# Optimization experiments

Hardware: AMD Instinct MI355X
Metric: run time of the kernel (lower is better)

The kernel has to match this reference:

```python
import jax, jax.numpy as jnp
import numpy as np

SEQ, B, I, H, STEPS = 512, 64, 512, 512, 5


def _lin_init(key, out_dim, in_dim):
    k1, k2 = jax.random.split(key)
    bound = 1.0 / np.sqrt(in_dim)
    W = jax.random.uniform(k1, (out_dim, in_dim), jnp.float32, -bound, bound)
    b = jax.random.uniform(k2, (out_dim,), jnp.float32, -bound, bound)
    return W, b


def _make_layer(key, in_size, hid):
    ks = jax.random.split(key, STEPS + 2)
    mogW, mogb = [], []
    for i in range(STEPS):
        # even i: Linear(hidden -> input) applied to h; odd i: Linear(input -> hidden) applied to x
        out_d, in_d = (in_size, hid) if i % 2 == 0 else (hid, in_size)
        W, b = _lin_init(ks[i], out_d, in_d)
        mogW.append(W); mogb.append(b)
    Wih, bih = _lin_init(ks[STEPS], 4 * hid, in_size)
    Whh, bhh = _lin_init(ks[STEPS + 1], 4 * hid, hid)
    return jnp.stack(mogW), jnp.stack(mogb), Wih, Whh, bih, bhh


def setup_inputs() -> dict:
    key = jax.random.key(0)
    kx, k1, k2 = jax.random.split(key, 3)
    inp = {"input_seq": jax.random.normal(kx, (SEQ, B, I), jnp.float32)}
    l1 = _make_layer(k1, I, H)
    l2 = _make_layer(k2, H, H)
    for pfx, p in (("l1", l1), ("l2", l2)):
        for nm, arr in zip(("mogW", "mogb", "Wih", "Whh", "bih", "bhh"), p):
            inp[f"{pfx}_{nm}"] = arr
    return inp


def _mog_cell(x, h, c, mogW, mogb, Wih, Whh, bih, bhh):
    # mogrify: 5 alternating gated linear updates
    for i in range(STEPS):
        if i % 2 == 0:
            x = 2.0 * jax.nn.sigmoid(h @ mogW[i].T + mogb[i]) * x
        else:
            h = 2.0 * jax.nn.sigmoid(x @ mogW[i].T + mogb[i]) * h
    # LSTMCell (PyTorch gate order: i, f, g, o)
    gates = x @ Wih.T + bih + h @ Whh.T + bhh
    ig, fg, gg, og = jnp.split(gates, 4, axis=-1)
    c = jax.nn.sigmoid(fg) * c + jax.nn.sigmoid(ig) * jnp.tanh(gg)
    h = jax.nn.sigmoid(og) * jnp.tanh(c)
    return h, c


def reference(input_seq, l1_mogW, l1_mogb, l1_Wih, l1_Whh, l1_bih, l1_bhh,
              l2_mogW, l2_mogb, l2_Wih, l2_Whh, l2_bih, l2_bhh):
    batch = input_seq.shape[1]
    h1 = jnp.zeros((batch, H), input_seq.dtype)
    c1 = jnp.zeros_like(h1); h2 = jnp.zeros_like(h1); c2 = jnp.zeros_like(h1)

    def step(carry, x_t):
        h1, c1, h2, c2 = carry
        h1, c1 = _mog_cell(x_t, h1, c1, l1_mogW, l1_mogb, l1_Wih, l1_Whh, l1_bih, l1_bhh)
        h2, c2 = _mog_cell(h1, h2, c2, l2_mogW, l2_mogb, l2_Wih, l2_Whh, l2_bih, l2_bhh)
        return (h1, c1, h2, c2), h2

    (h1, c1, h2, c2), outputs = jax.lax.scan(step, (h1, c1, h2, c2), input_seq)
    last_hidden = jnp.stack([h1, h2])  # [2, B, H]
    last_cell = jnp.stack([c1, c2])
    return outputs, last_hidden, last_cell
```

## Files before the change

kernel.cpp:

```cpp
#include <hip/hip_runtime.h>
#include <cstdint>

#define SEQ   512
#define BATCH 64
#define HID   512
#define BH    (BATCH*HID)
#define NWGP  32
#define NTHR  256

#define MOG_ELEMS   (5*512*512)
#define GATE_ELEMS  (2048*512)
#define LAYER_ELEMS (MOG_ELEMS + 2*GATE_ELEMS)

#define WS_FLG   0
#define WS_H16   4096
#define ZERO_PREFIX 266240
#define WS_X16   266240
#define WS_RING  397312
#define WS_WT    921600

#define OUT_H 16777216
#define OUT_C 16842752

typedef _Float16 f16x8 __attribute__((ext_vector_type(8)));
typedef float    f32x4 __attribute__((ext_vector_type(4)));

#define MFMA(a,b,c) __builtin_amdgcn_mfma_f32_16x16x32_f16((a),(b),(c),0,0,0)

#define GLD16(dst, ptr) \
    asm volatile("global_load_dwordx4 %0, %1, off sc0 sc1" : "=v"(dst) : "v"(ptr))
#define GLDF(dst, ptr) \
    asm volatile("global_load_dword %0, %1, off sc0 sc1" : "=v"(dst) : "v"(ptr))
#define GST16(ptr, val) \
    asm volatile("global_store_dwordx4 %0, %1, off sc0 sc1" :: "v"(ptr), "v"(val) : "memory")
#define FLAGST(ptr, val) \
    asm volatile("global_store_dword %0, %1, off sc0 sc1" :: "v"(ptr), "v"(val) : "memory")
#define VMWAIT() asm volatile("s_waitcnt vmcnt(0)" ::: "memory")

__device__ __forceinline__ float sigf(float z) { return 1.f / (1.f + __expf(-z)); }

__device__ __forceinline__ void poll_ge(const unsigned* line, unsigned tag) {
    if (threadIdx.x < 64) {
        const unsigned* p = line + (threadIdx.x & 31);
        for (;;) {
            unsigned v;
            asm volatile("global_load_dword %0, %1, off sc0 sc1\n\ts_waitcnt vmcnt(0)"
                         : "=v"(v) : "v"(p) : "memory");
            if (__ballot(v >= tag) == ~0ull) break;
        }
    }
    __syncthreads();
}

__device__ __forceinline__ int gate_orig_row(int rg) {
    return ((rg >> 4) & 3) * 512 + ((rg >> 6) << 4) + (rg & 15);
}

__global__ __launch_bounds__(256)
void prologue_convert(const float* __restrict__ l1_mogW, const float* __restrict__ l1_Wih,
                      const float* __restrict__ l1_Whh,
                      const float* __restrict__ l2_mogW, const float* __restrict__ l2_Wih,
                      const float* __restrict__ l2_Whh,  char* __restrict__ ws)
{
    _Float16* wdst = (_Float16*)(ws + WS_WT);
    const int total = 2 * LAYER_ELEMS;
    const int stride = gridDim.x * blockDim.x;
    for (int idx = blockIdx.x * blockDim.x + threadIdx.x; idx < total; idx += stride) {
        const int layer = idx >= LAYER_ELEMS;
        const int r = idx - layer * LAYER_ELEMS;
        float v;
        if (r < MOG_ELEMS) {
            v = (layer ? l2_mogW : l1_mogW)[r];
        } else {
            const int q = r - MOG_ELEMS;
            const int mat = q >= GATE_ELEMS;
            const int e = q - mat * GATE_ELEMS;
            const int rg = e >> 9;
            const int k  = e & 511;
            const int orig = gate_orig_row(rg);
            const float* W = mat ? (layer ? l2_Whh : l1_Whh)
                                 : (layer ? l2_Wih : l1_Wih);
            v = W[orig * 512 + k];
        }
        wdst[idx] = (_Float16)v;
    }
}

__global__ __launch_bounds__(NTHR, 1)
void moglstm_persist(const float* __restrict__ in_seq,
                     const float* __restrict__ mogb1, const float* __restrict__ mogb2,
                     const float* __restrict__ bih1,  const float* __restrict__ bhh1,
                     const float* __restrict__ bih2,  const float* __restrict__ bhh2,
                     float* __restrict__ out, char* __restrict__ ws)
{
    const int pool = blockIdx.x >> 5;
    const int w    = blockIdx.x & 31;
    const int tid  = threadIdx.x;
    const int lane = tid & 63;
    const int wv   = tid >> 6;

    extern __shared__ char smem[];
    _Float16* wlds = (_Float16*)smem;
    _Float16* hbuf = (_Float16*)(smem + 81920);
    float*    fbuf = (float*)(smem + 84992);

    unsigned* flg     = (unsigned*)(ws + WS_FLG);
    unsigned* myline  = flg + (pool * 6) * 32;
    unsigned* othline = flg + ((1 - pool) * 6) * 32;

    _Float16* h16 = (_Float16*)(ws + WS_H16) + pool * (2 * BH);
    _Float16* x16 = (_Float16*)(ws + WS_X16) + pool * BH;
    float*    ring = (float*)(ws + WS_RING);
    const _Float16* Wb   = (const _Float16*)(ws + WS_WT) + (size_t)pool * LAYER_ELEMS;
    const _Float16* mogW = Wb;
    const _Float16* wihR = Wb + MOG_ELEMS;
    const _Float16* whhR = wihR + GATE_ELEMS;
    const float* mogb = pool ? mogb2 : mogb1;
    const float* bih  = pool ? bih2 : bih1;
    const float* bhh  = pool ? bhh2 : bhh1;

    const int j     = lane & 15;
    const int hi    = lane >> 4;
    const int kof   = hi * 8;
    const int arow  = 16 * wv + j;
    const int erow0 = 16 * wv + 4 * hi;
    const int ecol  = 16 * w + j;
    const int cxor  = (j & 7) << 3;
    const int aoff  = (hi >> 1) * 1024 + arow * 16 + (hi & 1) * 8;

    for (int i = tid; i < 5 * 16 * 64; i += NTHR) {
        const int p   = i >> 10;
        const int rem = i & 1023;
        const int c   = rem >> 6;
        const int k   = (rem & 63) << 3;
        f16x8 v = *(const f16x8*)(mogW + ((size_t)p * 512 + 16 * w + c) * 512 + k);
        *(f16x8*)&wlds[((p * 16 + c) << 9) + (k ^ ((c & 7) << 3))] = v;
    }
    __syncthreads();

    float mb[5];
    #pragma unroll
    for (int p = 0; p < 5; ++p) mb[p] = mogb[p * 512 + ecol];
    float gbias[4];
    #pragma unroll
    for (int g = 0; g < 4; ++g) gbias[g] = bih[g * 512 + ecol] + bhh[g * 512 + ecol];

    float xreg[4];
    float hreg[4] = {0.f, 0.f, 0.f, 0.f};
    float creg[4] = {0.f, 0.f, 0.f, 0.f};

    for (int t = 0; t < SEQ; ++t) {
        _Float16* hb = h16 + (t & 1) * BH;
        _Float16* ho = h16 + ((t & 1) ^ 1) * BH;

        float xseq[4];
        if (pool == 0) {
            #pragma unroll
            for (int r = 0; r < 4; ++r)
                xseq[r] = in_seq[(size_t)t * BH + (erow0 + r) * HID + ecol];
        }

        #pragma unroll
        for (int p = 0; p < 5; ++p) {
            if (p == 0) {
                if (t > 0) poll_ge(myline + 5 * 32, 6u * (t - 1) + 6);
                if (pool == 1) poll_ge(othline + 5 * 32, 6u * t + 6);
            } else {
                poll_ge(myline + (p - 1) * 32, 6u * t + p);
            }

            const _Float16* act = (p & 1) ? x16 : hb;

            float rv[4];
            if (p == 0 && pool == 1) {
                const float* rp = ring + (t & 3) * BH + w * 1024 + erow0 * 16 + j;
                GLDF(rv[0], rp); GLDF(rv[1], rp + 16); GLDF(rv[2], rp + 32); GLDF(rv[3], rp + 48);
            }
            f16x8 a[16];
            {
                const _Float16* ab = act + aoff;
                #pragma unroll
                for (int ks = 0; ks < 16; ++ks) GLD16(a[ks], ab + ks * 2048);
            }
            VMWAIT();
            __builtin_amdgcn_sched_barrier(0);

            const _Float16* wl = wlds + ((p * 16 + j) << 9);
            f32x4 acc = {0.f, 0.f, 0.f, 0.f};
            #pragma unroll
            for (int ks = 0; ks < 16; ++ks)
                acc = MFMA(a[ks], *(const f16x8*)&wl[(kof + ks * 32) ^ cxor], acc);

            float nv[4];
            #pragma unroll
            for (int r = 0; r < 4; ++r) {
                const float s = 2.f * sigf(acc[r] + mb[p]);
                if ((p & 1) == 0) {
                    const float xo = (p == 0) ? ((pool == 0) ? xseq[r] : rv[r]) : xreg[r];
                    nv[r] = s * xo;  xreg[r] = nv[r];
                } else {
                    nv[r] = s * hreg[r];  hreg[r] = nv[r];
                }
            }
            _Float16* target = ((p & 1) == 0) ? x16 : hb;
            #pragma unroll
            for (int r = 0; r < 4; ++r) hbuf[(erow0 + r) * 24 + j] = (_Float16)nv[r];
            __syncthreads();
            if (tid < 128) {
                const int row = tid >> 1, c8 = (tid & 1) * 8;
                f16x8 v = *(const f16x8*)&hbuf[row * 24 + c8];
                GST16(target + w * 1024 + row * 16 + c8, v);
            }
            VMWAIT();
            __syncthreads();
            if (tid == 0) FLAGST(myline + p * 32 + w, 6u * t + p + 1);
        }

        poll_ge(myline + 4 * 32, 6u * t + 5);
        if (pool == 0 && t >= 4) poll_ge(othline + 0 * 32, 6u * (t - 4) + 1);

        f16x8 ax[16], ah[16];
        {
            const _Float16* xb = x16 + aoff;
            const _Float16* hB = hb  + aoff;
            #pragma unroll
            for (int ks = 0; ks < 16; ++ks) { GLD16(ax[ks], xb + ks * 2048); GLD16(ah[ks], hB + ks * 2048); }
        }
        VMWAIT();
        __builtin_amdgcn_sched_barrier(0);

        f32x4 g0 = {0,0,0,0}, g1 = {0,0,0,0}, g2 = {0,0,0,0}, g3 = {0,0,0,0};
        {
            const int n0 = 64 * w + j;
            const _Float16* bi0 = wihR + (size_t)(n0     ) * 512 + kof;
            const _Float16* bi1 = wihR + (size_t)(n0 + 16) * 512 + kof;
            const _Float16* bi2 = wihR + (size_t)(n0 + 32) * 512 + kof;
            const _Float16* bi3 = wihR + (size_t)(n0 + 48) * 512 + kof;
            const _Float16* bh0 = whhR + (size_t)(n0     ) * 512 + kof;
            const _Float16* bh1 = whhR + (size_t)(n0 + 16) * 512 + kof;
            const _Float16* bh2 = whhR + (size_t)(n0 + 32) * 512 + kof;
            const _Float16* bh3 = whhR + (size_t)(n0 + 48) * 512 + kof;
            #pragma unroll
            for (int ks = 0; ks < 16; ++ks) {
                const int o = ks * 32;
                g0 = MFMA(ax[ks], *(const f16x8*)(bi0 + o), g0);
                g0 = MFMA(ah[ks], *(const f16x8*)(bh0 + o), g0);
                g1 = MFMA(ax[ks], *(const f16x8*)(bi1 + o), g1);
                g1 = MFMA(ah[ks], *(const f16x8*)(bh1 + o), g1);
                g2 = MFMA(ax[ks], *(const f16x8*)(bi2 + o), g2);
                g2 = MFMA(ah[ks], *(const f16x8*)(bh2 + o), g2);
                g3 = MFMA(ax[ks], *(const f16x8*)(bi3 + o), g3);
                g3 = MFMA(ah[ks], *(const f16x8*)(bh3 + o), g3);
            }
        }
        float hnv[4], cnv[4];
        #pragma unroll
        for (int r = 0; r < 4; ++r) {
            const float ig = sigf (g0[r] + gbias[0]);
            const float fg = sigf (g1[r] + gbias[1]);
            const float gg = tanhf(g2[r] + gbias[2]);
            const float og = sigf (g3[r] + gbias[3]);
            const float cn = fg * creg[r] + ig * gg;
            creg[r] = cn;  cnv[r] = cn;
            const float hn = og * tanhf(cn);
            hreg[r] = hn;  hnv[r] = hn;
        }
        #pragma unroll
        for (int r = 0; r < 4; ++r) hbuf[(erow0 + r) * 24 + j] = (_Float16)hnv[r];
        if (pool == 0) {
            #pragma unroll
            for (int r = 0; r < 4; ++r) fbuf[(erow0 + r) * 20 + j] = hnv[r];
        } else {
            #pragma unroll
            for (int r = 0; r < 4; ++r)
                out[(size_t)t * BH + (erow0 + r) * HID + ecol] = hnv[r];
        }
        if (t == SEQ - 1) {
            #pragma unroll
            for (int r = 0; r < 4; ++r) {
                out[OUT_H + pool * BH + (erow0 + r) * HID + ecol] = hnv[r];
                out[OUT_C + pool * BH + (erow0 + r) * HID + ecol] = cnv[r];
            }
        }
        __syncthreads();
        if (tid < 128) {
            const int row = tid >> 1, c8 = (tid & 1) * 8;
            f16x8 v = *(const f16x8*)&hbuf[row * 24 + c8];
            GST16(ho + w * 1024 + row * 16 + c8, v);
        }
        if (pool == 0) {
            const int row = tid >> 2, c4 = (tid & 3) * 4;
            f32x4 v = *(const f32x4*)&fbuf[row * 20 + c4];
            GST16(ring + (t & 3) * BH + w * 1024 + row * 16 + c4, v);
        }
        VMWAIT();
        __syncthreads();
        if (tid == 0) FLAGST(myline + 5 * 32 + w, 6u * t + 6);
    }
}

extern "C" void kernel_launch(void* const* d_in, const int* in_sizes, int n_in,
                              void* d_out, int out_size, void* d_ws, size_t ws_size,
                              hipStream_t stream) {
    const float* in_seq  = (const float*)d_in[0];
    const float* l1_mogW = (const float*)d_in[1];
    const float* l1_mogb = (const float*)d_in[2];
    const float* l1_Wih  = (const float*)d_in[3];
    const float* l1_Whh  = (const float*)d_in[4];
    const float* l1_bih  = (const float*)d_in[5];
    const float* l1_bhh  = (const float*)d_in[6];
    const float* l2_mogW = (const float*)d_in[7];
    const float* l2_mogb = (const float*)d_in[8];
    const float* l2_Wih  = (const float*)d_in[9];
    const float* l2_Whh  = (const float*)d_in[10];
    const float* l2_bih  = (const float*)d_in[11];
    const float* l2_bhh  = (const float*)d_in[12];

    hipMemsetAsync(d_ws, 0, ZERO_PREFIX, stream);

    prologue_convert<<<256, 256, 0, stream>>>(l1_mogW, l1_Wih, l1_Whh,
                                              l2_mogW, l2_Wih, l2_Whh, (char*)d_ws);

    moglstm_persist<<<64, NTHR, 90112, stream>>>(in_seq, l1_mogb, l2_mogb,
                                                 l1_bih, l1_bhh, l2_bih, l2_bhh,
                                                 (float*)d_out, (char*)d_ws);
}
```

Before: 17.43 ms.

## Speculatively load activations while polling flags, split gate MFMAs across phases

Replaces the poll-then-syncthreads barrier with a loop in which every wave issues its activation loads together with the flag load, repeating until a poll after the flags are satisfied, so no separate barrier and load round trip is needed. Flags are spread to one per 64-byte slot (larger flag region, shifted workspace offsets). The recurrent Whh half of the LSTM gate GEMM is folded into the last mogrifier phase using the h already in registers, so the final stage only reloads x. Output stores become nontemporal. The extra speculative reload adds memory traffic, and correctness depends on the final load being ordered after the flag observation.

```diff
diff --git a/kernel.cpp b/kernel.cpp
--- a/kernel.cpp
+++ b/kernel.cpp
@@ -13,11 +13,11 @@
 #define LAYER_ELEMS (MOG_ELEMS + 2*GATE_ELEMS)
 
 #define WS_FLG   0
-#define WS_H16   4096
-#define ZERO_PREFIX 266240
-#define WS_X16   266240
-#define WS_RING  397312
-#define WS_WT    921600
+#define WS_H16   24576
+#define ZERO_PREFIX 286720
+#define WS_X16   286720
+#define WS_RING  417792
+#define WS_WT    942080
 
 #define OUT_H 16777216
 #define OUT_C 16842752
@@ -36,21 +36,12 @@
 #define FLAGST(ptr, val) \
     asm volatile("global_store_dword %0, %1, off sc0 sc1" :: "v"(ptr), "v"(val) : "memory")
 #define VMWAIT() asm volatile("s_waitcnt vmcnt(0)" ::: "memory")
+#define TIE(x)   asm volatile("" : "+v"(x))
+#define TAGLDW(dst, ptr) \
+    asm volatile("global_load_dword %0, %1, off sc0 sc1\n\ts_waitcnt vmcnt(0)" \
+                 : "=v"(dst) : "v"(ptr) : "memory")
 
 __device__ __forceinline__ float sigf(float z) { return 1.f / (1.f + __expf(-z)); }
-
-__device__ __forceinline__ void poll_ge(const unsigned* line, unsigned tag) {
-    if (threadIdx.x < 64) {
-        const unsigned* p = line + (threadIdx.x & 31);
-        for (;;) {
-            unsigned v;
-            asm volatile("global_load_dword %0, %1, off sc0 sc1\n\ts_waitcnt vmcnt(0)"
-                         : "=v"(v) : "v"(p) : "memory");
-            if (__ballot(v >= tag) == ~0ull) break;
-        }
-    }
-    __syncthreads();
-}
 
 __device__ __forceinline__ int gate_orig_row(int rg) {
     return ((rg >> 4) & 3) * 512 + ((rg >> 6) << 4) + (rg & 15);
@@ -104,9 +95,7 @@
     _Float16* hbuf = (_Float16*)(smem + 81920);
     float*    fbuf = (float*)(smem + 84992);
 
-    unsigned* flg     = (unsigned*)(ws + WS_FLG);
-    unsigned* myline  = flg + (pool * 6) * 32;
-    unsigned* othline = flg + ((1 - pool) * 6) * 32;
+    unsigned* flg = (unsigned*)(ws + WS_FLG);
 
     _Float16* h16 = (_Float16*)(ws + WS_H16) + pool * (2 * BH);
     _Float16* x16 = (_Float16*)(ws + WS_X16) + pool * BH;
@@ -128,6 +117,16 @@
     const int cxor  = (j & 7) << 3;
     const int aoff  = (hi >> 1) * 1024 + arow * 16 + (hi & 1) * 8;
 
+    const int n0 = 64 * w + j;
+    const _Float16* bi0 = wihR + (size_t)(n0     ) * 512 + kof;
+    const _Float16* bi1 = wihR + (size_t)(n0 + 16) * 512 + kof;
+    const _Float16* bi2 = wihR + (size_t)(n0 + 32) * 512 + kof;
+    const _Float16* bi3 = wihR + (size_t)(n0 + 48) * 512 + kof;
+    const _Float16* bh0 = whhR + (size_t)(n0     ) * 512 + kof;
+    const _Float16* bh1 = whhR + (size_t)(n0 + 16) * 512 + kof;
+    const _Float16* bh2 = whhR + (size_t)(n0 + 32) * 512 + kof;
+    const _Float16* bh3 = whhR + (size_t)(n0 + 48) * 512 + kof;
+
     for (int i = tid; i < 5 * 16 * 64; i += NTHR) {
         const int p   = i >> 10;
         const int rem = i & 1023;
@@ -148,10 +147,12 @@
     float xreg[4];
     float hreg[4] = {0.f, 0.f, 0.f, 0.f};
     float creg[4] = {0.f, 0.f, 0.f, 0.f};
+    f16x8 a[16];
 
     for (int t = 0; t < SEQ; ++t) {
         _Float16* hb = h16 + (t & 1) * BH;
         _Float16* ho = h16 + ((t & 1) ^ 1) * BH;
+        f32x4 g0 = {0,0,0,0}, g1 = {0,0,0,0}, g2 = {0,0,0,0}, g3 = {0,0,0,0};
 
         float xseq[4];
         if (pool == 0) {
@@ -162,27 +163,33 @@
 
         #pragma unroll
         for (int p = 0; p < 5; ++p) {
-            if (p == 0) {
-                if (t > 0) poll_ge(myline + 5 * 32, 6u * (t - 1) + 6);
-                if (pool == 1) poll_ge(othline + 5 * 32, 6u * t + 6);
-            } else {
-                poll_ge(myline + (p - 1) * 32, 6u * t + p);
-            }
+            const unsigned* prim = flg + (size_t)(pool * 6 + ((p == 0) ? 5 : p - 1)) * 512;
+            const unsigned* sec  = prim;
+            unsigned ptgt = 6u * (unsigned)t + (unsigned)p;
+            unsigned stgt = ptgt;
+            if (p == 0 && pool == 1) { sec = flg + (size_t)5 * 512; stgt = 6u * t + 6u; }
+            const unsigned* tp = (lane < 32) ? (prim + lane * 16) : (sec + (lane - 32) * 16);
+            const unsigned mytgt = (lane < 32) ? ptgt : stgt;
 
             const _Float16* act = (p & 1) ? x16 : hb;
-
+            const _Float16* ab  = act + aoff;
+            const float* rp = ring + (t & 3) * BH + w * 1024 + erow0 * 16 + j;
             float rv[4];
-            if (p == 0 && pool == 1) {
-                const float* rp = ring + (t & 3) * BH + w * 1024 + erow0 * 16 + j;
-                GLDF(rv[0], rp); GLDF(rv[1], rp + 16); GLDF(rv[2], rp + 32); GLDF(rv[3], rp + 48);
-            }
-            f16x8 a[16];
-            {
-                const _Float16* ab = act + aoff;
+            bool prev_ok = false;
+            for (;;) {
+                if (p == 0 && pool == 1) {
+                    GLDF(rv[0], rp); GLDF(rv[1], rp + 16); GLDF(rv[2], rp + 32); GLDF(rv[3], rp + 48);
+                }
                 #pragma unroll
                 for (int ks = 0; ks < 16; ++ks) GLD16(a[ks], ab + ks * 2048);
-            }
-            VMWAIT();
+                unsigned tagv;
+                TAGLDW(tagv, tp);
+                if (prev_ok) break;
+                prev_ok = (__ballot(tagv >= mytgt) == ~0ull);
+            }
+            #pragma unroll
+            for (int ks = 0; ks < 16; ++ks) TIE(a[ks]);
+            if (p == 0 && pool == 1) { TIE(rv[0]); TIE(rv[1]); TIE(rv[2]); TIE(rv[3]); }
             __builtin_amdgcn_sched_barrier(0);
 
             const _Float16* wl = wlds + ((p * 16 + j) << 9);
@@ -213,46 +220,54 @@
             }
             VMWAIT();
             __syncthreads();
-            if (tid == 0) FLAGST(myline + p * 32 + w, 6u * t + p + 1);
-        }
-
-        poll_ge(myline + 4 * 32, 6u * t + 5);
-        if (pool == 0 && t >= 4) poll_ge(othline + 0 * 32, 6u * (t - 4) + 1);
-
-        f16x8 ax[16], ah[16];
+            if (tid == 0) FLAGST(flg + (size_t)(pool * 6 + p) * 512 + w * 16, 6u * t + p + 1);
+
+            if (p == 4) {
+                #pragma unroll
+                for (int ks = 0; ks < 16; ++ks) {
+                    const int o = ks * 32;
+                    g0 = MFMA(a[ks], *(const f16x8*)(bh0 + o), g0);
+                    g1 = MFMA(a[ks], *(const f16x8*)(bh1 + o), g1);
+                    g2 = MFMA(a[ks], *(const f16x8*)(bh2 + o), g2);
+                    g3 = MFMA(a[ks], *(const f16x8*)(bh3 + o), g3);
+                }
+            }
+        }
+
         {
-            const _Float16* xb = x16 + aoff;
-            const _Float16* hB = hb  + aoff;
-            #pragma unroll
-            for (int ks = 0; ks < 16; ++ks) { GLD16(ax[ks], xb + ks * 2048); GLD16(ah[ks], hB + ks * 2048); }
-        }
-        VMWAIT();
-        __builtin_amdgcn_sched_barrier(0);
-
-        f32x4 g0 = {0,0,0,0}, g1 = {0,0,0,0}, g2 = {0,0,0,0}, g3 = {0,0,0,0};
-        {
-            const int n0 = 64 * w + j;
-            const _Float16* bi0 = wihR + (size_t)(n0     ) * 512 + kof;
-            const _Float16* bi1 = wihR + (size_t)(n0 + 16) * 512 + kof;
-            const _Float16* bi2 = wihR + (size_t)(n0 + 32) * 512 + kof;
-            const _Float16* bi3 = wihR + (size_t)(n0 + 48) * 512 + kof;
-            const _Float16* bh0 = whhR + (size_t)(n0     ) * 512 + kof;
-            const _Float16* bh1 = whhR + (size_t)(n0 + 16) * 512 + kof;
-            const _Float16* bh2 = whhR + (size_t)(n0 + 32) * 512 + kof;
-            const _Float16* bh3 = whhR + (size_t)(n0 + 48) * 512 + kof;
+            const unsigned* prim = flg + (size_t)(pool * 6 + 4) * 512;
+            const unsigned* sec  = prim;
+            unsigned ptgt = 6u * t + 5u;
+            unsigned stgt = ptgt;
+            if (pool == 0) { sec = flg + (size_t)(6 + 0) * 512;
+                             stgt = (t >= 4) ? (6u * (t - 4) + 1u) : 0u; }
+            const unsigned* tp = (lane < 32) ? (prim + lane * 16) : (sec + (lane - 32) * 16);
+            const unsigned mytgt = (lane < 32) ? ptgt : stgt;
+
+            const _Float16* ab = x16 + aoff;
+            bool prev_ok = false;
+            for (;;) {
+                #pragma unroll
+                for (int ks = 0; ks < 16; ++ks) GLD16(a[ks], ab + ks * 2048);
+                unsigned tagv;
+                TAGLDW(tagv, tp);
+                if (prev_ok) break;
+                prev_ok = (__ballot(tagv >= mytgt) == ~0ull);
+            }
+            #pragma unroll
+            for (int ks = 0; ks < 16; ++ks) TIE(a[ks]);
+            __builtin_amdgcn_sched_barrier(0);
+
             #pragma unroll
             for (int ks = 0; ks < 16; ++ks) {
                 const int o = ks * 32;
-                g0 = MFMA(ax[ks], *(const f16x8*)(bi0 + o), g0);
-                g0 = MFMA(ah[ks], *(const f16x8*)(bh0 + o), g0);
-                g1 = MFMA(ax[ks], *(const f16x8*)(bi1 + o), g1);
-                g1 = MFMA(ah[ks], *(const f16x8*)(bh1 + o), g1);
-                g2 = MFMA(ax[ks], *(const f16x8*)(bi2 + o), g2);
-                g2 = MFMA(ah[ks], *(const f16x8*)(bh2 + o), g2);
-                g3 = MFMA(ax[ks], *(const f16x8*)(bi3 + o), g3);
-                g3 = MFMA(ah[ks], *(const f16x8*)(bh3 + o), g3);
-            }
-        }
+                g0 = MFMA(a[ks], *(const f16x8*)(bi0 + o), g0);
+                g1 = MFMA(a[ks], *(const f16x8*)(bi1 + o), g1);
+                g2 = MFMA(a[ks], *(const f16x8*)(bi2 + o), g2);
+                g3 = MFMA(a[ks], *(const f16x8*)(bi3 + o), g3);
+            }
+        }
+
         float hnv[4], cnv[4];
         #pragma unroll
         for (int r = 0; r < 4; ++r) {
@@ -273,13 +288,13 @@
         } else {
             #pragma unroll
             for (int r = 0; r < 4; ++r)
-                out[(size_t)t * BH + (erow0 + r) * HID + ecol] = hnv[r];
+                __builtin_nontemporal_store(hnv[r], &out[(size_t)t * BH + (erow0 + r) * HID + ecol]);
         }
         if (t == SEQ - 1) {
             #pragma unroll
             for (int r = 0; r < 4; ++r) {
-                out[OUT_H + pool * BH + (erow0 + r) * HID + ecol] = hnv[r];
-                out[OUT_C + pool * BH + (erow0 + r) * HID + ecol] = cnv[r];
+                __builtin_nontemporal_store(hnv[r], &out[OUT_H + pool * BH + (erow0 + r) * HID + ecol]);
+                __builtin_nontemporal_store(cnv[r], &out[OUT_C + pool * BH + (erow0 + r) * HID + ecol]);
             }
         }
         __syncthreads();
@@ -295,7 +310,7 @@
         }
         VMWAIT();
         __syncthreads();
-        if (tid == 0) FLAGST(myline + 5 * 32 + w, 6u * t + 6);
+        if (tid == 0) FLAGST(flg + (size_t)(pool * 6 + 5) * 512 + w * 16, 6u * t + 6u);
     }
 }
 
```

New measurement: 16.16 ms. 1.08x faster.
